# Optimization experiments

Measured on AMD Instinct MI355X. Metric: run time of the kernel, lower is better.

## Reference

```python
import jax, jax.numpy as jnp
import numpy as np

I = 8    # num invariants (max_invariants)
IL = 4   # objects (variables) per invariant
BL = 25  # objects per batch example
P1 = 64  # unary predicates
P2 = 16  # binary predicates
B = 64   # batch size
ALPHA = 0.999


def _others_index(n):
    # others[i, j] = index of the j-th object != i, in order (skip i).
    j = np.arange(n - 1)[None, :]
    i = np.arange(n)[:, None]
    return jnp.asarray(j + (j >= i))  # (n, n-1) int


def reduce_probsum(x, axis=-1):
    # probabilistic OR: 1 - prod(1 - x)
    return 1.0 - jnp.prod(1.0 - x, axis=axis)


def softmax_scale(size, alpha=ALPHA):
    # static python-int size, matches tf.cond(size == 1, ...)
    if size == 1:
        return 1.0
    return float(np.log(alpha * (size - 1) / (1.0 - alpha)))


def unify(inv_unary_conds, inv_binary_conds, unary_feats, binary_feats, iterations=1):
    # inv_unary_conds (I, IL, P1), inv_binary_conds (I, IL, IL-1, P2)
    # unary_feats (B, BL, P1), binary_feats (B, BL, BL-1, P2)
    # Unary match: prob that object o satisfies all unary conds of variable v -> (B, I, IL, BL)
    t1 = jnp.prod(
        1.0 - inv_unary_conds[None, :, :, None, :] * (1.0 - unary_feats[:, None, None, :, :]),
        axis=-1,
    )
    # Binary match for (v, v') against (o, o') -> (B, I, IL, IL-1, BL, BL-1)
    t2 = jnp.prod(
        1.0
        - inv_binary_conds[None, :, :, :, None, None, :]
        * (1.0 - binary_feats[:, None, None, None, :, :, :]),
        axis=-1,
    )
    vothers = _others_index(inv_unary_conds.shape[1])  # (IL, IL-1)
    oothers = _others_index(unary_feats.shape[1])      # (BL, BL-1)
    uni = t1
    for _ in range(iterations):
        # Current map gathered at partner pairs (v', o'): (B, I, IL, IL-1, BL, BL-1)
        ug = uni[:, :, vothers, :][..., oothers]
        # OR over partner objects o', AND over partner variables v' -> (B, I, IL, BL)
        bsat = jnp.prod(reduce_probsum(ug * t2, axis=-1), axis=3)
        uni = t1 * bsat
    return uni  # (B, I, IL, BL)


def setup_inputs() -> dict:
    key = jax.random.key(0)
    ks = jax.random.split(key, 6)
    inp = {
        'inv_unary_feats': jax.random.uniform(ks[0], (I, IL, P1), dtype=jnp.float32),
        'inv_binary_feats': jax.random.uniform(ks[1], (I, IL, IL - 1, P2), dtype=jnp.float32),
        'unary_feats': jax.random.uniform(ks[2], (B, BL, P1), dtype=jnp.float32),
        'binary_feats': jax.random.uniform(ks[3], (B, BL, BL - 1, P2), dtype=jnp.float32),
        # RandomNormal(mean=-1, stddev=0.05) initializer from build()
        'inv_unaryp': -1.0 + 0.05 * jax.random.normal(ks[4], (I, IL, P1), dtype=jnp.float32),
        'inv_binaryp': -1.0 + 0.05 * jax.random.normal(ks[5], (I, IL, IL - 1, P2), dtype=jnp.float32),
    }
    return inp


def reference(inv_unary_feats, inv_binary_feats, unary_feats, binary_feats, inv_unaryp, inv_binaryp):
    num_invs = inv_unary_feats.shape[0]
    inv_unary_map = jax.nn.sigmoid(inv_unaryp[:num_invs])
    inv_binary_map = jax.nn.sigmoid(inv_binaryp[:num_invs])
    inv_unary_conds = inv_unary_map * inv_unary_feats    # (I, IL, P1)
    inv_binary_conds = inv_binary_map * inv_binary_feats  # (I, IL, IL-1, P2)
    uni_sets = unify(inv_unary_conds, inv_binary_conds, unary_feats, binary_feats, iterations=1)
    # OR over batch objects, AND over invariant objects -> (B, I)
    inv_uni = jnp.prod(reduce_probsum(uni_sets, axis=-1), axis=-1)
    inv_select = jax.nn.softmax(inv_uni * softmax_scale(num_invs), axis=-1)
    return uni_sets, inv_select
```

## Files before the change

### kernel.cpp

```cpp
#include <hip/hip_runtime.h>
#include <math.h>

#define NI 8
#define IL 4
#define BL 25
#define P1 64
#define P2 16
#define NB 64

#define CUF_STRIDE 65
#define CBF_STRIDE 392

__global__ __launch_bounds__(320) void unify_kernel(
    const float* __restrict__ inv_unary_feats,
    const float* __restrict__ inv_binary_feats,
    const float* __restrict__ unary_feats,
    const float* __restrict__ binary_feats,
    const float* __restrict__ inv_unaryp,
    const float* __restrict__ inv_binaryp,
    float* __restrict__ out_uni,
    float* __restrict__ inv_uni_ws)
{
    __shared__ float cuf_s[BL * CUF_STRIDE];
    __shared__ float cbf_s[BL * CBF_STRIDE];
    __shared__ float uc_s[IL * 65];
    __shared__ float bc_s[IL * 3 * P2];
    __shared__ float t1_s[IL * BL];
    __shared__ float P_s[BL * 12];
    __shared__ float uni_s[IL * BL];
    __shared__ float ps_s[IL];

    const int bid = blockIdx.x;
    const int b = bid >> 3;
    const int i = bid & 7;
    const int t = threadIdx.x;

    if (t < IL * P1) {
        int v = t >> 6, p = t & 63;
        float pr = inv_unaryp[i * IL * P1 + t];
        float s = 1.0f / (1.0f + expf(-pr));
        uc_s[v * 65 + p] = s * inv_unary_feats[i * IL * P1 + t];
    }
    if (t < IL * 3 * P2) {
        float pr = inv_binaryp[i * IL * 3 * P2 + t];
        float s = 1.0f / (1.0f + expf(-pr));
        bc_s[t] = s * inv_binary_feats[i * IL * 3 * P2 + t];
    }
    for (int idx = t; idx < BL * P1; idx += 320) {
        int o = idx >> 6, p = idx & 63;
        cuf_s[o * CUF_STRIDE + p] = 1.0f - unary_feats[b * BL * P1 + idx];
    }
    {
        const float4* src4 = reinterpret_cast<const float4*>(binary_feats + (size_t)b * BL * 24 * P2);
        float4* dst4 = reinterpret_cast<float4*>(cbf_s);
        for (int idx = t; idx < BL * 24 * P2 / 4; idx += 320) {
            int o = idx / 96, r = idx - o * 96;
            float4 x = src4[idx];
            float4 y;
            y.x = 1.0f - x.x; y.y = 1.0f - x.y; y.z = 1.0f - x.z; y.w = 1.0f - x.w;
            dst4[o * (CBF_STRIDE / 4) + r] = y;
        }
    }
    __syncthreads();

    if (t < IL * BL) {
        int v = t / BL, o = t - v * BL;
        const float* ucv = uc_s + v * 65;
        const float* cufo = cuf_s + o * CUF_STRIDE;
        float a0 = 1.f, a1 = 1.f, a2 = 1.f, a3 = 1.f;
#pragma unroll
        for (int p = 0; p < P1; p += 4) {
            a0 *= fmaf(-ucv[p],     cufo[p],     1.f);
            a1 *= fmaf(-ucv[p + 1], cufo[p + 1], 1.f);
            a2 *= fmaf(-ucv[p + 2], cufo[p + 2], 1.f);
            a3 *= fmaf(-ucv[p + 3], cufo[p + 3], 1.f);
        }
        t1_s[t] = (a0 * a1) * (a2 * a3);
    }
    __syncthreads();

    if (t < BL * 12) {
        int o = t / 12;
        int j = t - o * 12;
        int v = j / 3;
        int vp = j - v * 3;
        int w = vp + (vp >= v ? 1 : 0);

        const float4* bc4 = reinterpret_cast<const float4*>(bc_s + j * P2);
        float4 q0 = bc4[0], q1 = bc4[1], q2 = bc4[2], q3 = bc4[3];

        const float* t1w = t1_s + w * BL;
        const float* co = cbf_s + o * CBF_STRIDE;

        float prodP = 1.0f;
#pragma unroll
        for (int op = 0; op < 24; ++op) {
            int oo = op + (op >= o ? 1 : 0);
            float tg = t1w[oo];
            const float4* c4 = reinterpret_cast<const float4*>(co + op * P2);
            float4 c0 = c4[0], c1 = c4[1], c2 = c4[2], c3 = c4[3];
            float p0 = fmaf(-q0.x, c0.x, 1.f) * fmaf(-q0.y, c0.y, 1.f);
            float p1 = fmaf(-q0.z, c0.z, 1.f) * fmaf(-q0.w, c0.w, 1.f);
            float p2 = fmaf(-q1.x, c1.x, 1.f) * fmaf(-q1.y, c1.y, 1.f);
            float p3 = fmaf(-q1.z, c1.z, 1.f) * fmaf(-q1.w, c1.w, 1.f);
            float p4 = fmaf(-q2.x, c2.x, 1.f) * fmaf(-q2.y, c2.y, 1.f);
            float p5 = fmaf(-q2.z, c2.z, 1.f) * fmaf(-q2.w, c2.w, 1.f);
            float p6 = fmaf(-q3.x, c3.x, 1.f) * fmaf(-q3.y, c3.y, 1.f);
            float p7 = fmaf(-q3.z, c3.z, 1.f) * fmaf(-q3.w, c3.w, 1.f);
            float t2 = ((p0 * p1) * (p2 * p3)) * ((p4 * p5) * (p6 * p7));
            prodP *= fmaf(-tg, t2, 1.0f);
        }
        P_s[t] = prodP;
    }
    __syncthreads();

    if (t < IL * BL) {
        int v = t / BL, o = t - v * BL;
        int base = o * 12 + v * 3;
        float bsat = (1.0f - P_s[base]) * (1.0f - P_s[base + 1]) * (1.0f - P_s[base + 2]);
        float u = t1_s[t] * bsat;
        uni_s[t] = u;
        out_uni[(size_t)bid * (IL * BL) + t] = u;
    }
    __syncthreads();

    if (t < IL) {
        const float* uv = uni_s + t * BL;
        float pv = 1.0f;
#pragma unroll
        for (int o = 0; o < BL; ++o) pv *= (1.0f - uv[o]);
        ps_s[t] = 1.0f - pv;
    }
    __syncthreads();
    if (t == 0) {
        inv_uni_ws[bid] = (ps_s[0] * ps_s[1]) * (ps_s[2] * ps_s[3]);
    }
}

__global__ __launch_bounds__(64) void softmax_kernel(
    const float* __restrict__ inv_uni,
    float* __restrict__ out)
{
    int b = threadIdx.x;
    const float S = logf(0.999f * 7.0f / (1.0f - 0.999f));
    float x[NI];
    float m = -3.0e38f;
#pragma unroll
    for (int k = 0; k < NI; ++k) {
        x[k] = inv_uni[b * NI + k];
        m = fmaxf(m, x[k]);
    }
    float s = 0.0f;
#pragma unroll
    for (int k = 0; k < NI; ++k) {
        x[k] = expf((x[k] - m) * S);
        s += x[k];
    }
    float inv = 1.0f / s;
#pragma unroll
    for (int k = 0; k < NI; ++k) out[b * NI + k] = x[k] * inv;
}

extern "C" void kernel_launch(void* const* d_in, const int* in_sizes, int n_in,
                              void* d_out, int out_size, void* d_ws, size_t ws_size,
                              hipStream_t stream) {
    const float* inv_unary_feats  = (const float*)d_in[0];
    const float* inv_binary_feats = (const float*)d_in[1];
    const float* unary_feats      = (const float*)d_in[2];
    const float* binary_feats     = (const float*)d_in[3];
    const float* inv_unaryp       = (const float*)d_in[4];
    const float* inv_binaryp      = (const float*)d_in[5];

    float* out = (float*)d_out;
    float* inv_uni_ws = (float*)d_ws;

    unify_kernel<<<NB * NI, 320, 0, stream>>>(
        inv_unary_feats, inv_binary_feats, unary_feats, binary_feats,
        inv_unaryp, inv_binaryp, out, inv_uni_ws);

    softmax_kernel<<<1, 64, 0, stream>>>(inv_uni_ws, out + (size_t)NB * NI * IL * BL);
}
```

Measured before the change: 85.31 us.

## Fuse softmax into unify kernel via sentinel-flagged cross-block spin wait

Removes the separate softmax kernel. Each block publishes its per-invariant score to workspace with a release atomic store, and the block handling the last invariant of each batch example spin-waits on sentinel values for its siblings, then computes the softmax itself. A tiny init kernel writes the sentinels each call. This trades one tail launch for an extra init launch plus a cross-block dependency that could deadlock if sibling blocks are not co-resident. The wait uses relaxed loads without an acquire.

```diff
diff --git a/kernel.cpp b/kernel.cpp
--- a/kernel.cpp
+++ b/kernel.cpp
@@ -11,15 +11,21 @@
 #define CUF_STRIDE 65
 #define CBF_STRIDE 392
 
-__global__ __launch_bounds__(320) void unify_kernel(
+#define SENTINEL 0xAAAAAAAAu
+
+__global__ __launch_bounds__(512) void init_ws_kernel(unsigned int* __restrict__ vals_ws) {
+    vals_ws[threadIdx.x] = SENTINEL;
+}
+
+__global__ __launch_bounds__(320) void unify_fused_kernel(
     const float* __restrict__ inv_unary_feats,
     const float* __restrict__ inv_binary_feats,
     const float* __restrict__ unary_feats,
     const float* __restrict__ binary_feats,
     const float* __restrict__ inv_unaryp,
     const float* __restrict__ inv_binaryp,
-    float* __restrict__ out_uni,
-    float* __restrict__ inv_uni_ws)
+    float* __restrict__ out,
+    unsigned int* __restrict__ vals_ws)
 {
     __shared__ float cuf_s[BL * CUF_STRIDE];
     __shared__ float cbf_s[BL * CBF_STRIDE];
@@ -120,7 +126,7 @@
         float bsat = (1.0f - P_s[base]) * (1.0f - P_s[base + 1]) * (1.0f - P_s[base + 2]);
         float u = t1_s[t] * bsat;
         uni_s[t] = u;
-        out_uni[(size_t)bid * (IL * BL) + t] = u;
+        out[(size_t)bid * (IL * BL) + t] = u;
     }
     __syncthreads();
 
@@ -132,33 +138,38 @@
         ps_s[t] = 1.0f - pv;
     }
     __syncthreads();
+
     if (t == 0) {
-        inv_uni_ws[bid] = (ps_s[0] * ps_s[1]) * (ps_s[2] * ps_s[3]);
+        float myval = (ps_s[0] * ps_s[1]) * (ps_s[2] * ps_s[3]);
+        __hip_atomic_store(&vals_ws[bid], __float_as_uint(myval),
+                           __ATOMIC_RELEASE, __HIP_MEMORY_SCOPE_AGENT);
+        if (i == 7) {
+            float x[NI];
+#pragma unroll
+            for (int k = 0; k < NI; ++k) {
+                unsigned int u;
+                do {
+                    u = __hip_atomic_load(&vals_ws[b * NI + k],
+                                          __ATOMIC_RELAXED, __HIP_MEMORY_SCOPE_AGENT);
+                } while (u == SENTINEL);
+                x[k] = __uint_as_float(u);
+            }
+            const float S = logf(0.999f * 7.0f / (1.0f - 0.999f));
+            float m = x[0];
+#pragma unroll
+            for (int k = 1; k < NI; ++k) m = fmaxf(m, x[k]);
+            float s = 0.0f;
+#pragma unroll
+            for (int k = 0; k < NI; ++k) {
+                x[k] = expf((x[k] - m) * S);
+                s += x[k];
+            }
+            float inv = 1.0f / s;
+            float* sel = out + (size_t)NB * NI * IL * BL + b * NI;
+#pragma unroll
+            for (int k = 0; k < NI; ++k) sel[k] = x[k] * inv;
+        }
     }
-}
-
-__global__ __launch_bounds__(64) void softmax_kernel(
-    const float* __restrict__ inv_uni,
-    float* __restrict__ out)
-{
-    int b = threadIdx.x;
-    const float S = logf(0.999f * 7.0f / (1.0f - 0.999f));
-    float x[NI];
-    float m = -3.0e38f;
-#pragma unroll
-    for (int k = 0; k < NI; ++k) {
-        x[k] = inv_uni[b * NI + k];
-        m = fmaxf(m, x[k]);
-    }
-    float s = 0.0f;
-#pragma unroll
-    for (int k = 0; k < NI; ++k) {
-        x[k] = expf((x[k] - m) * S);
-        s += x[k];
-    }
-    float inv = 1.0f / s;
-#pragma unroll
-    for (int k = 0; k < NI; ++k) out[b * NI + k] = x[k] * inv;
 }
 
 extern "C" void kernel_launch(void* const* d_in, const int* in_sizes, int n_in,
@@ -172,11 +183,11 @@
     const float* inv_binaryp      = (const float*)d_in[5];
 
     float* out = (float*)d_out;
-    float* inv_uni_ws = (float*)d_ws;
+    unsigned int* vals_ws = (unsigned int*)d_ws;
 
-    unify_kernel<<<NB * NI, 320, 0, stream>>>(
+    init_ws_kernel<<<1, NB * NI, 0, stream>>>(vals_ws);
+
+    unify_fused_kernel<<<NB * NI, 320, 0, stream>>>(
         inv_unary_feats, inv_binary_feats, unary_feats, binary_feats,
-        inv_unaryp, inv_binaryp, out, inv_uni_ws);
-
-    softmax_kernel<<<1, 64, 0, stream>>>(inv_uni_ws, out + (size_t)NB * NI * IL * BL);
+        inv_unaryp, inv_binaryp, out, vals_ws);
 }
```

Result: slower. 90.64 us (+6.3%).
